# Kernel optimization log

Hardware: AMD Instinct MI355X
Metric: run time of the kernel (lower is better)

Reference implementation:

```python
import jax, jax.numpy as jnp
import numpy as np

B, N, C, HEADS, R = 8, 4096, 256, 8, 4  # N = H*W, R = reduction_ratio
LN_EPS = 1e-5


def setup_inputs() -> dict:
    key = jax.random.key(0)
    ks = jax.random.split(key, 6)
    sc = 0.02
    return {
        "x": jax.random.normal(ks[0], (B, N, C), jnp.float32),
        "conv_w": jax.random.normal(ks[1], (C, C, R, R), jnp.float32) * sc,  # OIHW
        "conv_b": jnp.zeros((C,), jnp.float32),
        "ln_g": jnp.ones((C,), jnp.float32),
        "ln_b": jnp.zeros((C,), jnp.float32),
        "kv_w": jax.random.normal(ks[2], (2 * C, C), jnp.float32) * sc,  # torch Linear (out,in)
        "kv_b": jnp.zeros((2 * C,), jnp.float32),
        "q_w": jax.random.normal(ks[3], (C, C), jnp.float32) * sc,
        "q_b": jnp.zeros((C,), jnp.float32),
        "out_w": jax.random.normal(ks[4], (C, C), jnp.float32) * sc,
        "out_b": jnp.zeros((C,), jnp.float32),
        "H": 64,
        "W": 64,
    }


def reference(x, conv_w, conv_b, ln_g, ln_b, kv_w, kv_b, q_w, q_b, out_w, out_b, H, W):
    Bz, Nq, Ch = x.shape
    d = Ch // HEADS
    scale = 1.0 / np.sqrt(float(d)).astype(np.float32)

    # spatial reduction: (B,N,C) -> (B,C,H,W) -> strided conv -> (B, M, C)
    x1 = x.transpose(0, 2, 1).reshape(Bz, Ch, H, W)
    x1 = jax.lax.conv_general_dilated(
        x1, conv_w, window_strides=(R, R), padding="VALID",
        dimension_numbers=("NCHW", "OIHW", "NCHW"))
    x1 = x1 + conv_b[None, :, None, None]
    x1 = x1.reshape(Bz, Ch, -1).transpose(0, 2, 1)  # (B, M, C), M=(H/R)*(W/R)

    # LayerNorm over channels
    mu = x1.mean(-1, keepdims=True)
    var = x1.var(-1, keepdims=True)
    x1 = (x1 - mu) / jnp.sqrt(var + LN_EPS) * ln_g + ln_b

    # K,V from reduced tokens
    kv = x1 @ kv_w.T + kv_b                                  # (B, M, 2C)
    M = kv.shape[1]
    kv = kv.reshape(Bz, M, 2, HEADS, d).transpose(2, 0, 3, 1, 4)  # (2,B,h,M,d)
    k, v = kv[0], kv[1]

    # Q from full-resolution tokens
    q = (x @ q_w.T + q_b).reshape(Bz, Nq, HEADS, d).transpose(0, 2, 1, 3)  # (B,h,N,d)

    attn = jax.nn.softmax(jnp.einsum("bhnd,bhmd->bhnm", q, k) * scale, axis=-1)
    out = jnp.einsum("bhnm,bhmd->bhnd", attn, v)             # (B,h,N,d)
    out = out.transpose(0, 2, 1, 3).reshape(Bz, Nq, Ch)
    return out @ out_w.T + out_b
```

## Files before the change

kernel.cpp:

```cpp
#include <hip/hip_runtime.h>
#include <math.h>

#define LN_EPS 1e-5f
#define SCALE_QK 0.17677669529663687f

using bf16x8 = __bf16 __attribute__((ext_vector_type(8)));
using f32x4 = float __attribute__((ext_vector_type(4)));

__device__ __forceinline__ ushort f2bf(float f) {
  unsigned u = __float_as_uint(f);
  u += 0x7fff + ((u >> 16) & 1);
  return (ushort)(u >> 16);
}

__device__ __forceinline__ void gload_lds16(const ushort* g, ushort* l) {
  __builtin_amdgcn_global_load_lds((__attribute__((address_space(1))) void*)g,
                                   (__attribute__((address_space(3))) void*)l, 16, 0, 0);
}

__global__ __launch_bounds__(256) void prep_kernel(
    const float* __restrict__ x, ushort* __restrict__ xb,
    const float* __restrict__ qw, const float* __restrict__ kvw,
    const float* __restrict__ ow, const float* __restrict__ cw,
    ushort* __restrict__ qwb, ushort* __restrict__ kvwb,
    ushort* __restrict__ owb, ushort* __restrict__ wTb) {
  int blk = blockIdx.x, tid = threadIdx.x;
  if (blk < 2048) {
    int i = blk * 1024 + tid;
#pragma unroll
    for (int p = 0; p < 4; ++p) {
      float4 v = ((const float4*)x)[i + p * 256];
      ushort4 o = {f2bf(v.x), f2bf(v.y), f2bf(v.z), f2bf(v.w)};
      ((ushort4*)xb)[i + p * 256] = o;
    }
  } else if (blk < 2304) {
    int b2 = blk - 2048;
    const float* src;
    ushort* dst;
    int i;
    if (b2 < 64) { src = qw; dst = qwb; i = b2 * 256 + tid; }
    else if (b2 < 192) { src = kvw; dst = kvwb; i = (b2 - 64) * 256 + tid; }
    else { src = ow; dst = owb; i = (b2 - 192) * 256 + tid; }
    float4 v = ((const float4*)src)[i];
    ushort4 o = {f2bf(v.x), f2bf(v.y), f2bf(v.z), f2bf(v.w)};
    ((ushort4*)dst)[i] = o;
  } else {
    int oc = blk - 2304, ic = tid;
    const float* src = cw + (size_t)oc * 4096 + ic * 16;
#pragma unroll
    for (int pos = 0; pos < 16; ++pos)
      wTb[(size_t)oc * 4096 + pos * 256 + ic] = f2bf(src[pos]);
  }
}

template <bool CONV, bool BIAS, int OUTMODE>
__global__ __launch_bounds__(256) void mfma_gemm(const ushort* __restrict__ A,
                                                 const ushort* __restrict__ Bw,
                                                 const float* __restrict__ bias,
                                                 float* __restrict__ C,
                                                 ushort* __restrict__ aux,
                                                 ushort* __restrict__ aux2, int Kld,
                                                 int Kslice, int Nld, size_t zstride) {
  __shared__ __attribute__((aligned(16))) ushort As[128 * 32];
  __shared__ __attribute__((aligned(16))) ushort Bs[64 * 32];
  int tid = threadIdx.x;
  int lane = tid & 63, w = tid >> 6;
  int m0 = blockIdx.y * 128, n0 = blockIdx.x * 64;
  int kbase = blockIdx.z * Kslice;
  int arow0 = w * 16 + (lane >> 2);
  int acol = (lane & 3) * 8;
  f32x4 acc[2][4];
#pragma unroll
  for (int i = 0; i < 2; ++i)
#pragma unroll
    for (int j = 0; j < 4; ++j) acc[i][j] = (f32x4){0.f, 0.f, 0.f, 0.f};

  for (int k0 = 0; k0 < Kslice; k0 += 32) {
    int kg = kbase + k0;
    __syncthreads();
#pragma unroll
    for (int t = 0; t < 2; ++t) {
      int row = arow0 + t * 64;
      const ushort* src;
      if (CONV) {
        int m = m0 + row;
        int b = m >> 8, mm = m & 255;
        int oh = mm >> 4, ow = mm & 15;
        int k = kg + acol;
        int pos = k >> 8, ic = k & 255;
        int n = ((oh << 2) + (pos >> 2)) * 64 + (ow << 2) + (pos & 3);
        src = A + ((size_t)(b * 4096 + n) * 256 + ic);
      } else {
        src = A + ((size_t)(m0 + row) * Kld + kg + acol);
      }
      gload_lds16(src, &As[t * 2048 + w * 512]);
    }
    {
      const ushort* srcb = Bw + ((size_t)(n0 + w * 16 + (lane >> 2)) * Kld + kg + acol);
      gload_lds16(srcb, &Bs[w * 512]);
    }
    __syncthreads();
    int qk = (lane >> 4) * 8, l15 = lane & 15;
    bf16x8 a0 = *(const bf16x8*)&As[(w * 32 + l15) * 32 + qk];
    bf16x8 a1 = *(const bf16x8*)&As[(w * 32 + 16 + l15) * 32 + qk];
#pragma unroll
    for (int j = 0; j < 4; ++j) {
      bf16x8 bj = *(const bf16x8*)&Bs[(j * 16 + l15) * 32 + qk];
      acc[0][j] = __builtin_amdgcn_mfma_f32_16x16x32_bf16(a0, bj, acc[0][j], 0, 0, 0);
      acc[1][j] = __builtin_amdgcn_mfma_f32_16x16x32_bf16(a1, bj, acc[1][j], 0, 0, 0);
    }
  }
  int l15 = lane & 15, q = lane >> 4;
  if (OUTMODE == 0) {
    float* Cz = C + (size_t)blockIdx.z * zstride;
#pragma unroll
    for (int i = 0; i < 2; ++i) {
#pragma unroll
      for (int j = 0; j < 4; ++j) {
        int col = n0 + j * 16 + l15;
        float bv = BIAS ? bias[col] : 0.f;
#pragma unroll
        for (int r = 0; r < 4; ++r) {
          int row = m0 + w * 32 + i * 16 + q * 4 + r;
          Cz[(size_t)row * Nld + col] = acc[i][j][r] + bv;
        }
      }
    }
  } else {
#pragma unroll
    for (int i = 0; i < 2; ++i) {
      int rowb = m0 + w * 32 + i * 16 + q * 4;
      int b = rowb >> 8, mloc = rowb & 255;
#pragma unroll
      for (int j = 0; j < 4; ++j) {
        int col = n0 + j * 16 + l15;
        float bv = bias[col];
        if (col < 256) {
#pragma unroll
          for (int r = 0; r < 4; ++r)
            aux[(size_t)(b * 256 + mloc + r) * 256 + col] = f2bf(acc[i][j][r] + bv);
        } else {
          int c2 = col - 256, h = c2 >> 5, d = c2 & 31;
          unsigned lo = (unsigned)f2bf(acc[i][j][0] + bv) |
                        ((unsigned)f2bf(acc[i][j][1] + bv) << 16);
          unsigned hi = (unsigned)f2bf(acc[i][j][2] + bv) |
                        ((unsigned)f2bf(acc[i][j][3] + bv) << 16);
          *(uint2*)(aux2 + ((size_t)((b * 8 + h) * 32 + d) * 256 + mloc)) =
              make_uint2(lo, hi);
        }
      }
    }
  }
}

template <bool F32OUT>
__global__ __launch_bounds__(256, 2) void breg_gemm(const ushort* __restrict__ A,
                                                    const ushort* __restrict__ Bw,
                                                    const float* __restrict__ bias,
                                                    float* __restrict__ Cf,
                                                    ushort* __restrict__ Cb) {
  int tid = threadIdx.x, lane = tid & 63, w = tid >> 6;
  int l15 = lane & 15, quad = lane >> 4;
  int n0 = blockIdx.x * 64;
  int m0 = blockIdx.y * 256 + w * 64;
  bf16x8 bfr[4][8];
  const ushort* bbase = Bw + (size_t)(n0 + l15) * 256 + quad * 8;
#pragma unroll
  for (int j = 0; j < 4; ++j)
#pragma unroll
    for (int kc = 0; kc < 8; ++kc)
      bfr[j][kc] = *(const bf16x8*)(bbase + (size_t)j * 16 * 256 + kc * 32);
  float bv[4];
#pragma unroll
  for (int j = 0; j < 4; ++j) bv[j] = bias[n0 + j * 16 + l15];

#pragma unroll
  for (int t = 0; t < 4; ++t) {
    const ushort* arow = A + (size_t)(m0 + t * 16 + l15) * 256 + quad * 8;
    bf16x8 af[8];
#pragma unroll
    for (int kc = 0; kc < 8; ++kc) af[kc] = *(const bf16x8*)(arow + kc * 32);
    f32x4 acc[4];
#pragma unroll
    for (int j = 0; j < 4; ++j) acc[j] = (f32x4){0.f, 0.f, 0.f, 0.f};
#pragma unroll
    for (int kc = 0; kc < 8; ++kc)
#pragma unroll
      for (int j = 0; j < 4; ++j)
        acc[j] = __builtin_amdgcn_mfma_f32_16x16x32_bf16(af[kc], bfr[j][kc], acc[j], 0, 0, 0);
#pragma unroll
    for (int j = 0; j < 4; ++j)
#pragma unroll
      for (int r = 0; r < 4; ++r) {
        int row = m0 + t * 16 + quad * 4 + r;
        int col = n0 + j * 16 + l15;
        float vv = acc[j][r] + bv[j];
        if (F32OUT) Cf[(size_t)row * 256 + col] = vv;
        else Cb[(size_t)row * 256 + col] = f2bf(vv);
      }
  }
}

__global__ __launch_bounds__(256) void ln_fused(const float* __restrict__ part,
                                                const float* __restrict__ cb,
                                                const float* __restrict__ g,
                                                const float* __restrict__ bt,
                                                ushort* __restrict__ x1b) {
  int t = blockIdx.x, c = threadIdx.x;
  size_t idx = (size_t)t * 256 + c;
  float v = cb[c];
#pragma unroll
  for (int z = 0; z < 8; ++z) v += part[idx + (size_t)z * 524288];
  float s1 = v, s2 = v * v;
#pragma unroll
  for (int o = 32; o > 0; o >>= 1) {
    s1 += __shfl_down(s1, o, 64);
    s2 += __shfl_down(s2, o, 64);
  }
  __shared__ float r1[4], r2[4];
  __shared__ float mu_s, rstd_s;
  int wv = c >> 6, lane = c & 63;
  if (lane == 0) { r1[wv] = s1; r2[wv] = s2; }
  __syncthreads();
  if (c == 0) {
    float S1 = r1[0] + r1[1] + r1[2] + r1[3];
    float S2 = r2[0] + r2[1] + r2[2] + r2[3];
    float mu = S1 * (1.f / 256.f);
    float var = S2 * (1.f / 256.f) - mu * mu;
    mu_s = mu;
    rstd_s = rsqrtf(var + LN_EPS);
  }
  __syncthreads();
  x1b[idx] = f2bf((v - mu_s) * rstd_s * g[c] + bt[c]);
}

__global__ __launch_bounds__(256) void attn_mfma(const ushort* __restrict__ qbb,
                                                 const ushort* __restrict__ kb,
                                                 const ushort* __restrict__ vT,
                                                 ushort* __restrict__ aob) {
  __shared__ __attribute__((aligned(16))) ushort P[4][16 * 264];
  int bid = blockIdx.x;
  int chunk = bid & 15, h = (bid >> 4) & 7, b = bid >> 7;
  int tid = threadIdx.x, lane = tid & 63, w = tid >> 6;
  int l15 = lane & 15, quad = lane >> 4;
  ushort* Pw = &P[w][0];

  bf16x8 kf[16];
  const ushort* kbase = kb + ((size_t)(b * 256 + l15)) * 256 + h * 32 + quad * 8;
#pragma unroll
  for (int mt = 0; mt < 16; ++mt)
    kf[mt] = *(const bf16x8*)(kbase + (size_t)mt * 16 * 256);
  bf16x8 vf[2][8];
  const ushort* vbase = vT + (size_t)(b * 8 + h) * 32 * 256;
#pragma unroll
  for (int j = 0; j < 2; ++j)
#pragma unroll
    for (int kc = 0; kc < 8; ++kc)
      vf[j][kc] = *(const bf16x8*)(vbase + (size_t)(j * 16 + l15) * 256 + kc * 32 + quad * 8);

  const float Cc = SCALE_QK * 1.4426950408889634f;
  int q0base = b * 4096 + chunk * 256 + w * 64;
  const ushort* qptr = qbb + (size_t)(q0base + l15) * 256 + h * 32 + quad * 8;

  bf16x8 qn = *(const bf16x8*)qptr;
  for (int t = 0; t < 4; ++t) {
    bf16x8 qf = qn;
    if (t < 3) qn = *(const bf16x8*)(qptr + (size_t)(t + 1) * 16 * 256);
    int q0 = q0base + t * 16;
    float lsum = 0.f;
#pragma unroll
    for (int mt = 0; mt < 16; ++mt) {
      f32x4 st = __builtin_amdgcn_mfma_f32_16x16x32_bf16(
          kf[mt], qf, (f32x4){0.f, 0.f, 0.f, 0.f}, 0, 0, 0);
      unsigned u[4];
#pragma unroll
      for (int r = 0; r < 4; ++r) {
        float e = exp2f(st[r] * Cc);
        unsigned ur = (__float_as_uint(e) + 0x8000u) & 0xffff0000u;
        lsum += __uint_as_float(ur);
        u[r] = ur;
      }
      unsigned lo = (u[0] >> 16) | u[1];
      unsigned hi = (u[2] >> 16) | u[3];
      *(uint2*)(Pw + l15 * 264 + mt * 16 + quad * 4) = make_uint2(lo, hi);
    }
    lsum += __shfl_xor(lsum, 16, 64);
    lsum += __shfl_xor(lsum, 32, 64);
    __threadfence_block();
    f32x4 oacc[2] = {{0.f, 0.f, 0.f, 0.f}, {0.f, 0.f, 0.f, 0.f}};
#pragma unroll
    for (int kc = 0; kc < 8; ++kc) {
      bf16x8 pf = *(const bf16x8*)(Pw + l15 * 264 + kc * 32 + quad * 8);
      oacc[0] = __builtin_amdgcn_mfma_f32_16x16x32_bf16(pf, vf[0][kc], oacc[0], 0, 0, 0);
      oacc[1] = __builtin_amdgcn_mfma_f32_16x16x32_bf16(pf, vf[1][kc], oacc[1], 0, 0, 0);
    }
    float linv[4];
#pragma unroll
    for (int r = 0; r < 4; ++r) linv[r] = 1.0f / __shfl(lsum, quad * 4 + r, 64);
    ushort* ob = aob + (size_t)q0 * 256 + h * 32;
#pragma unroll
    for (int j = 0; j < 2; ++j)
#pragma unroll
      for (int r = 0; r < 4; ++r) {
        unsigned uo = __float_as_uint(oacc[j][r] * linv[r]) + 0x8000u;
        ob[(size_t)(quad * 4 + r) * 256 + j * 16 + l15] = (ushort)(uo >> 16);
      }
  }
}

extern "C" void kernel_launch(void* const* d_in, const int* in_sizes, int n_in,
                              void* d_out, int out_size, void* d_ws, size_t ws_size,
                              hipStream_t stream) {
  const float* x = (const float*)d_in[0];
  const float* conv_w = (const float*)d_in[1];
  const float* conv_b = (const float*)d_in[2];
  const float* ln_g = (const float*)d_in[3];
  const float* ln_b = (const float*)d_in[4];
  const float* kv_w = (const float*)d_in[5];
  const float* kv_b = (const float*)d_in[6];
  const float* q_w = (const float*)d_in[7];
  const float* q_b = (const float*)d_in[8];
  const float* out_w = (const float*)d_in[9];
  const float* out_b = (const float*)d_in[10];

  ushort* xb = (ushort*)d_ws;
  ushort* wTb = xb + 8388608;
  ushort* qwb = wTb + 1048576;
  ushort* kvwb = qwb + 65536;
  ushort* owb = kvwb + 131072;
  ushort* x1b = owb + 65536;
  ushort* kb = x1b + 524288;
  ushort* vT = kb + 524288;
  ushort* aob = xb;
  float* part = (float*)d_out;
  ushort* qbb = (ushort*)((float*)d_out + 4194304);

  prep_kernel<<<2560, 256, 0, stream>>>(x, xb, q_w, kv_w, out_w, conv_w,
                                        qwb, kvwb, owb, wTb);
  mfma_gemm<true, false, 0><<<dim3(4, 16, 8), 256, 0, stream>>>(
      xb, wTb, nullptr, part, nullptr, nullptr, 4096, 512, 256, 524288);
  ln_fused<<<2048, 256, 0, stream>>>(part, conv_b, ln_g, ln_b, x1b);
  mfma_gemm<false, true, 2><<<dim3(8, 16, 1), 256, 0, stream>>>(
      x1b, kvwb, kv_b, nullptr, kb, vT, 256, 256, 512, 0);
  breg_gemm<false><<<dim3(4, 128), 256, 0, stream>>>(xb, qwb, q_b, nullptr, qbb);
  attn_mfma<<<1024, 256, 0, stream>>>(qbb, kb, vT, aob);
  breg_gemm<true><<<dim3(4, 128), 256, 0, stream>>>(aob, owb, out_b, (float*)d_out, nullptr);
}
```

Baseline: 216.7 us.

## Stage K/V tiles via LDS async loads, use raw exp2 and lighter fence

Each wave now cooperatively copies its share of the K and V tiles into shared memory using global_load_lds. Fragments are then read from LDS, so there are no redundant per-lane strided global loads of K and V. The softmax switches to the hardware exp2 builtin and sums unrounded exponentials. It also replaces the block threadfence with an explicit LDS waitcnt and drops the Q prefetch in favour of a per-iteration load. The change adds two block barriers and reuses the shared buffer for P, and the lsum now differs slightly from the rounded P values.

```diff
diff --git a/kernel.cpp b/kernel.cpp
--- a/kernel.cpp
+++ b/kernel.cpp
@@ -238,35 +238,44 @@
                                                  const ushort* __restrict__ kb,
                                                  const ushort* __restrict__ vT,
                                                  ushort* __restrict__ aob) {
-  __shared__ __attribute__((aligned(16))) ushort P[4][16 * 264];
+  __shared__ __attribute__((aligned(16))) ushort sh[4 * 16 * 264];
   int bid = blockIdx.x;
   int chunk = bid & 15, h = (bid >> 4) & 7, b = bid >> 7;
   int tid = threadIdx.x, lane = tid & 63, w = tid >> 6;
   int l15 = lane & 15, quad = lane >> 4;
-  ushort* Pw = &P[w][0];
-
+
+  {
+    const ushort* srcK = kb + (size_t)(b * 256 + w * 64 + (lane >> 2)) * 256 +
+                         h * 32 + (lane & 3) * 8;
+#pragma unroll
+    for (int i = 0; i < 4; ++i)
+      gload_lds16(srcK + (size_t)i * 16 * 256, &sh[(w * 64 + i * 16) * 32]);
+    const ushort* srcV = vT + (size_t)((b * 8 + h) * 32 + w * 8 + (lane >> 5)) * 256 +
+                         (lane & 31) * 8;
+#pragma unroll
+    for (int i = 0; i < 4; ++i)
+      gload_lds16(srcV + (size_t)i * 2 * 256, &sh[8192 + (w * 8 + i * 2) * 256]);
+  }
+  __syncthreads();
   bf16x8 kf[16];
-  const ushort* kbase = kb + ((size_t)(b * 256 + l15)) * 256 + h * 32 + quad * 8;
 #pragma unroll
   for (int mt = 0; mt < 16; ++mt)
-    kf[mt] = *(const bf16x8*)(kbase + (size_t)mt * 16 * 256);
+    kf[mt] = *(const bf16x8*)&sh[(mt * 16 + l15) * 32 + quad * 8];
   bf16x8 vf[2][8];
-  const ushort* vbase = vT + (size_t)(b * 8 + h) * 32 * 256;
 #pragma unroll
   for (int j = 0; j < 2; ++j)
 #pragma unroll
     for (int kc = 0; kc < 8; ++kc)
-      vf[j][kc] = *(const bf16x8*)(vbase + (size_t)(j * 16 + l15) * 256 + kc * 32 + quad * 8);
+      vf[j][kc] = *(const bf16x8*)&sh[8192 + (j * 16 + l15) * 256 + kc * 32 + quad * 8];
+  __syncthreads();
+  ushort* Pw = &sh[w * 16 * 264];
 
   const float Cc = SCALE_QK * 1.4426950408889634f;
   int q0base = b * 4096 + chunk * 256 + w * 64;
-  const ushort* qptr = qbb + (size_t)(q0base + l15) * 256 + h * 32 + quad * 8;
-
-  bf16x8 qn = *(const bf16x8*)qptr;
+
   for (int t = 0; t < 4; ++t) {
-    bf16x8 qf = qn;
-    if (t < 3) qn = *(const bf16x8*)(qptr + (size_t)(t + 1) * 16 * 256);
     int q0 = q0base + t * 16;
+    bf16x8 qf = *(const bf16x8*)(qbb + (size_t)(q0 + l15) * 256 + h * 32 + quad * 8);
     float lsum = 0.f;
 #pragma unroll
     for (int mt = 0; mt < 16; ++mt) {
@@ -275,18 +284,17 @@
       unsigned u[4];
 #pragma unroll
       for (int r = 0; r < 4; ++r) {
-        float e = exp2f(st[r] * Cc);
-        unsigned ur = (__float_as_uint(e) + 0x8000u) & 0xffff0000u;
-        lsum += __uint_as_float(ur);
-        u[r] = ur;
-      }
-      unsigned lo = (u[0] >> 16) | u[1];
-      unsigned hi = (u[2] >> 16) | u[3];
+        float e = __builtin_amdgcn_exp2f(st[r] * Cc);
+        lsum += e;
+        u[r] = __float_as_uint(e) + 0x8000u;
+      }
+      unsigned lo = (u[0] >> 16) | (u[1] & 0xffff0000u);
+      unsigned hi = (u[2] >> 16) | (u[3] & 0xffff0000u);
       *(uint2*)(Pw + l15 * 264 + mt * 16 + quad * 4) = make_uint2(lo, hi);
     }
     lsum += __shfl_xor(lsum, 16, 64);
     lsum += __shfl_xor(lsum, 32, 64);
-    __threadfence_block();
+    __builtin_amdgcn_s_waitcnt(0xc07f);
     f32x4 oacc[2] = {{0.f, 0.f, 0.f, 0.f}, {0.f, 0.f, 0.f, 0.f}};
 #pragma unroll
     for (int kc = 0; kc < 8; ++kc) {
```

Measured after the change: 206.0 us. -5.0%, faster.
